# Kernel tuning notes

Hardware: AMD Instinct MI355X
Metric: run time of the kernel (lower is better)

The kernel has to match this reference:

```python
import jax, jax.numpy as jnp
import numpy as np

B, T, D, M = 64, 2048, 256, 20
UNIT = 2
RADIUS_FACTOR = 0.2
SIGMA_FACTOR = 0.2
KERNEL = 3
TOPK = 100
EPS = 1e-12


def setup_inputs() -> dict:
    key = jax.random.key(0)
    ks = jax.random.split(key, 10)
    x = jax.random.normal(ks[0], (B, T, D), jnp.float32)
    saliency = jax.random.normal(ks[1], (B, T), jnp.float32)
    # ground-truth boundaries in frame units, -1 start marks padding objects
    b0 = jax.random.uniform(ks[2], (B, M), minval=0.0, maxval=UNIT * (T - 100))
    length = jax.random.uniform(ks[3], (B, M), minval=UNIT * 2.0, maxval=UNIT * 100.0)
    b1 = jnp.minimum(b0 + length, float(UNIT * T))
    valid = jax.random.uniform(ks[4], (B, M)) < 0.8
    b0 = jnp.where(valid, b0, -1.0)
    boundary = jnp.stack([b0, b1], axis=-1)
    sc = 1.0 / np.sqrt(D)
    w_center = jax.random.normal(ks[5], (D, 1), jnp.float32) * sc
    w_window = jax.random.normal(ks[6], (D, 1), jnp.float32) * sc
    w_offset = jax.random.normal(ks[7], (D, 1), jnp.float32) * sc
    zb = jnp.zeros((1,), jnp.float32)
    return dict(x=x, w_center=w_center, b_center=zb, w_window=w_window, b_window=zb,
                w_offset=w_offset, b_offset=zb, saliency=saliency, boundary=boundary)


def _get_targets(boundary):
    # boundary: [B, M, 2] in frame units; vectorized version of the torch double loop
    b0 = boundary[..., 0]
    b1 = boundary[..., 1]
    valid = b0 != -1.0                                   # [B, M]
    b0c = b0 / UNIT
    b1c = (b1 - UNIT) / UNIT
    centers = jnp.minimum((b0c + b1c) * 0.5, T - 0.5)    # [B, M]
    windows = b1c - b0c                                   # [B, M]
    radius = (windows * RADIUS_FACTOR).astype(jnp.int32)  # trunc like .int()
    sigma = (radius.astype(jnp.float32) + 1.0) * SIGMA_FACTOR
    ci = centers.astype(jnp.int32)                        # [B, M]
    t = jnp.arange(T)
    d = t[None, None, :] - ci[..., None]                  # [B, M, T]
    g = jnp.exp(-(d.astype(jnp.float32) ** 2) / (2.0 * sigma[..., None] ** 2))
    inband = (jnp.abs(d) <= radius[..., None]) & valid[..., None]
    g = jnp.where(inband, g, 0.0)
    center_tgt = g.max(axis=1)                            # scatter-max over objects
    rows = jnp.arange(B)[:, None]
    idx = jnp.where(valid, ci, T)                         # out-of-range -> dropped
    z = jnp.zeros((B, T), jnp.float32)
    window_tgt = z.at[rows, idx].set(windows, mode='drop')
    offset_tgt = z.at[rows, idx].set(centers - ci.astype(jnp.float32), mode='drop')
    weight = z.at[rows, idx].set(1.0, mode='drop')
    avg_factor = valid.sum().astype(jnp.float32)
    return center_tgt, window_tgt, offset_tgt, weight, avg_factor


def _get_boundary(center_pred, window_pred, offset_pred):
    pad = (KERNEL - 1) // 2
    hmax = jax.lax.reduce_window(center_pred, -jnp.inf, jax.lax.max,
                                 (1, KERNEL), (1, 1), [(0, 0), (pad, pad)])
    cp = jnp.where(hmax == center_pred, center_pred, 0.0)
    scores, inds = jax.lax.top_k(cp, TOPK)                # [B, TOPK]
    off = jnp.maximum(jnp.take_along_axis(offset_pred, inds, axis=1), 0.0)
    center = inds.astype(jnp.float32) + off
    window = jnp.maximum(jnp.take_along_axis(window_pred, inds, axis=1), 0.0)
    lo = jnp.clip(center - window / 2, 0.0, T - 1.0) * UNIT
    hi = jnp.clip(center + window / 2, 0.0, T - 1.0) * UNIT + UNIT
    return jnp.stack([lo, hi, scores], axis=-1)           # [B, TOPK, 3]


def reference(x, w_center, b_center, w_window, b_window, w_offset, b_offset, saliency, boundary):
    mask = (saliency >= 0).astype(x.dtype)                # [B, T]
    center_pred = jax.nn.sigmoid(jnp.einsum('btd,do->bt', x, w_center) + b_center[0]) * mask
    window_pred = jnp.einsum('btd,do->bt', x, w_window) + b_window[0]
    offset_pred = jnp.einsum('btd,do->bt', x, w_offset) + b_offset[0]

    center_tgt, window_tgt, offset_tgt, weight, avg = _get_targets(boundary)

    # GaussianFocalLoss (alpha=2, gamma=4), weighted by mask, mean over avg_factor
    pos = (center_tgt == 1.0).astype(jnp.float32)
    pos_loss = -jnp.log(center_pred + EPS) * (1.0 - center_pred) ** 2 * pos
    neg_loss = -jnp.log(1.0 - center_pred + EPS) * center_pred ** 2 * (1.0 - center_tgt) ** 4
    center_loss = ((pos_loss + neg_loss) * mask).sum() / avg
    window_loss = 0.1 * (jnp.abs(window_pred - window_tgt) * weight).sum() / avg
    offset_loss = 1.0 * (jnp.abs(offset_pred - offset_tgt) * weight).sum() / avg

    boundary_out = _get_boundary(center_pred, window_pred, offset_pred)
    return (boundary_out, center_loss, window_loss, offset_loss)
```

## Files before the change

### kernel.cpp

```cpp
#include <hip/hip_runtime.h>
#include <math.h>

#define BB 64
#define TT 2048
#define DD 256
#define MM 20
#define TOPK_N 100
#define EPSF 1e-12f

__global__ __launch_bounds__(256) void preds_kernel(
    const float* __restrict__ x,
    const float* __restrict__ wc, const float* __restrict__ bc,
    const float* __restrict__ ww, const float* __restrict__ bw,
    const float* __restrict__ wo, const float* __restrict__ bo,
    const float* __restrict__ sal,
    float* __restrict__ cp, float* __restrict__ wp, float* __restrict__ op)
{
    const int lane = threadIdx.x & 63;
    const int waveg = blockIdx.x * 4 + (threadIdx.x >> 6);
    const int nwaves = gridDim.x * 4;

    const float4 wc4 = ((const float4*)wc)[lane];
    const float4 ww4 = ((const float4*)ww)[lane];
    const float4 wo4 = ((const float4*)wo)[lane];
    const float bcs = bc[0], bws = bw[0], bos = bo[0];

    for (int row = waveg; row < BB * TT; row += nwaves) {
        const float4 x4 = ((const float4*)(x + (size_t)row * DD))[lane];
        float sc = x4.x * wc4.x + x4.y * wc4.y + x4.z * wc4.z + x4.w * wc4.w;
        float sw = x4.x * ww4.x + x4.y * ww4.y + x4.z * ww4.z + x4.w * ww4.w;
        float so = x4.x * wo4.x + x4.y * wo4.y + x4.z * wo4.z + x4.w * wo4.w;
        #pragma unroll
        for (int m = 32; m >= 1; m >>= 1) {
            sc += __shfl_xor(sc, m, 64);
            sw += __shfl_xor(sw, m, 64);
            so += __shfl_xor(so, m, 64);
        }
        if (lane == 0) {
            const float mask = (sal[row] >= 0.0f) ? 1.0f : 0.0f;
            const float z = sc + bcs;
            const float s = 1.0f / (1.0f + expf(-z));
            cp[row] = s * mask;
            wp[row] = sw + bws;
            op[row] = so + bos;
        }
    }
}

__global__ __launch_bounds__(256) void targets_kernel(
    const float* __restrict__ boundary, const float* __restrict__ sal,
    const float* __restrict__ cp, const float* __restrict__ wp,
    const float* __restrict__ op, float* __restrict__ partials)
{
    __shared__ int   s_ci[MM];
    __shared__ float s_win[MM], s_off[MM], s_sig[MM];
    __shared__ int   s_rad[MM], s_valid[MM], s_last[MM];
    __shared__ float s_red[4][4];

    const int b = blockIdx.x;
    const int tid = threadIdx.x;

    if (tid < MM) {
        const float b0 = boundary[(b * MM + tid) * 2 + 0];
        const float b1 = boundary[(b * MM + tid) * 2 + 1];
        const int v = (b0 != -1.0f) ? 1 : 0;
        const float b0c = b0 * 0.5f;
        const float b1c = (b1 - 2.0f) * 0.5f;
        const float c = fminf((b0c + b1c) * 0.5f, (float)TT - 0.5f);
        const float w = b1c - b0c;
        const int r = (int)(w * 0.2f);
        const float sg = ((float)r + 1.0f) * 0.2f;
        const int ci = (int)c;
        s_ci[tid] = ci; s_win[tid] = w; s_off[tid] = c - (float)ci;
        s_sig[tid] = sg; s_rad[tid] = r; s_valid[tid] = v;
    }
    __syncthreads();
    if (tid < MM) {
        int last = s_valid[tid];
        if (last) {
            for (int m2 = tid + 1; m2 < MM; ++m2)
                if (s_valid[m2] && s_ci[m2] == s_ci[tid]) { last = 0; break; }
        }
        s_last[tid] = last;
    }
    __syncthreads();

    float cl = 0.0f, wl = 0.0f, ol = 0.0f, cnt = 0.0f;
    if (tid < MM) {
        if (s_valid[tid]) cnt = 1.0f;
        if (s_last[tid]) {
            const int t = s_ci[tid];
            wl = fabsf(wp[b * TT + t] - s_win[tid]);
            ol = fabsf(op[b * TT + t] - s_off[tid]);
        }
    }
    for (int t = tid; t < TT; t += 256) {
        float ctgt = 0.0f;
        for (int m = 0; m < MM; ++m) {
            if (!s_valid[m]) continue;
            const int d = t - s_ci[m];
            const int ad = d < 0 ? -d : d;
            if (ad <= s_rad[m]) {
                const float df = (float)d;
                const float sg = s_sig[m];
                const float g = expf(-(df * df) / (2.0f * sg * sg));
                ctgt = fmaxf(ctgt, g);
            }
        }
        const float p = cp[b * TT + t];
        const float mask = (sal[b * TT + t] >= 0.0f) ? 1.0f : 0.0f;
        const float pos = (ctgt == 1.0f) ? 1.0f : 0.0f;
        const float om = 1.0f - p;
        const float pl = -logf(p + EPSF) * om * om * pos;
        const float q = 1.0f - ctgt;
        const float q2 = q * q;
        const float nl = -logf(1.0f - p + EPSF) * p * p * (q2 * q2);
        cl += (pl + nl) * mask;
    }
    #pragma unroll
    for (int m = 32; m >= 1; m >>= 1) {
        cl  += __shfl_xor(cl,  m, 64);
        wl  += __shfl_xor(wl,  m, 64);
        ol  += __shfl_xor(ol,  m, 64);
        cnt += __shfl_xor(cnt, m, 64);
    }
    if ((tid & 63) == 0) {
        const int w = tid >> 6;
        s_red[w][0] = cl; s_red[w][1] = wl; s_red[w][2] = ol; s_red[w][3] = cnt;
    }
    __syncthreads();
    if (tid == 0) {
        float a = 0, b2 = 0, c = 0, d = 0;
        for (int w = 0; w < 4; ++w) {
            a += s_red[w][0]; b2 += s_red[w][1]; c += s_red[w][2]; d += s_red[w][3];
        }
        partials[b * 4 + 0] = a; partials[b * 4 + 1] = b2;
        partials[b * 4 + 2] = c; partials[b * 4 + 3] = d;
    }
}

__global__ void finalize_kernel(const float* __restrict__ partials, float* __restrict__ out)
{
    if (threadIdx.x == 0 && blockIdx.x == 0) {
        float cl = 0, wl = 0, ol = 0, cnt = 0;
        for (int i = 0; i < BB; ++i) {
            cl += partials[i * 4 + 0]; wl += partials[i * 4 + 1];
            ol += partials[i * 4 + 2]; cnt += partials[i * 4 + 3];
        }
        out[BB * TOPK_N * 3 + 0] = cl / cnt;
        out[BB * TOPK_N * 3 + 1] = 0.1f * wl / cnt;
        out[BB * TOPK_N * 3 + 2] = ol / cnt;
    }
}

__global__ __launch_bounds__(256) void topk_kernel(
    const float* __restrict__ cp, const float* __restrict__ wp,
    const float* __restrict__ op, float* __restrict__ out)
{
    __shared__ unsigned long long keys[TT];
    const int b = blockIdx.x;
    const int tid = threadIdx.x;
    const float* row = cp + b * TT;

    for (int t = tid; t < TT; t += 256) {
        const float p = row[t];
        const float l = (t > 0) ? row[t - 1] : -1.0f;
        const float r = (t < TT - 1) ? row[t + 1] : -1.0f;
        const float hm = fmaxf(p, fmaxf(l, r));
        const float v = (hm == p) ? p : 0.0f;
        keys[t] = ((unsigned long long)__float_as_uint(v) << 32)
                | (unsigned int)(0xFFFFFFFFu - (unsigned int)t);
    }
    __syncthreads();

    for (int k = 2; k <= TT; k <<= 1) {
        for (int j = k >> 1; j >= 1; j >>= 1) {
            for (int i = tid; i < TT; i += 256) {
                const int p = i ^ j;
                if (p > i) {
                    const bool desc = ((i & k) == 0);
                    const unsigned long long a = keys[i], bk = keys[p];
                    const bool sw = desc ? (a < bk) : (a > bk);
                    if (sw) { keys[i] = bk; keys[p] = a; }
                }
            }
            __syncthreads();
        }
    }

    if (tid < TOPK_N) {
        const unsigned long long kk = keys[tid];
        const int idx = (int)(0xFFFFFFFFu - (unsigned int)kk);
        const float score = __uint_as_float((unsigned int)(kk >> 32));
        const float off = fmaxf(op[b * TT + idx], 0.0f);
        const float center = (float)idx + off;
        const float win = fmaxf(wp[b * TT + idx], 0.0f);
        const float lo = fminf(fmaxf(center - win * 0.5f, 0.0f), (float)TT - 1.0f) * 2.0f;
        const float hi = fminf(fmaxf(center + win * 0.5f, 0.0f), (float)TT - 1.0f) * 2.0f + 2.0f;
        float* o = out + (b * TOPK_N + tid) * 3;
        o[0] = lo; o[1] = hi; o[2] = score;
    }
}

extern "C" void kernel_launch(void* const* d_in, const int* in_sizes, int n_in,
                              void* d_out, int out_size, void* d_ws, size_t ws_size,
                              hipStream_t stream) {
    const float* x   = (const float*)d_in[0];
    const float* wc  = (const float*)d_in[1];
    const float* bc  = (const float*)d_in[2];
    const float* ww  = (const float*)d_in[3];
    const float* bw  = (const float*)d_in[4];
    const float* wo  = (const float*)d_in[5];
    const float* bo  = (const float*)d_in[6];
    const float* sal = (const float*)d_in[7];
    const float* bnd = (const float*)d_in[8];
    float* out = (float*)d_out;

    float* ws = (float*)d_ws;
    float* cp = ws;
    float* wp = ws + BB * TT;
    float* op = ws + 2 * BB * TT;
    float* partials = ws + 3 * BB * TT;

    preds_kernel<<<4096, 256, 0, stream>>>(x, wc, bc, ww, bw, wo, bo, sal, cp, wp, op);
    targets_kernel<<<BB, 256, 0, stream>>>(bnd, sal, cp, wp, op, partials);
    finalize_kernel<<<1, 64, 0, stream>>>(partials, out);
    topk_kernel<<<BB, 256, 0, stream>>>(cp, wp, op, out);
}
```

Before: 294.8 us.

## Process four rows per wave in preds, fold finalize into topk, widen topk blocks

The projection kernel now assigns four rows per wavefront, with 16 lanes per row each loading four float4 chunks. This cuts the shuffle reduction from six steps to four and gives each lane more independent loads in flight. The separate finalize kernel is removed and its loss reduction moves into block 0 of the top-k kernel as a wave-level shuffle reduction, saving one launch. The top-k bitonic sort now runs with 512 threads per block instead of 256, halving the per-thread work in each sort pass.

```diff
diff --git a/kernel.cpp b/kernel.cpp
--- a/kernel.cpp
+++ b/kernel.cpp
@@ -17,29 +17,41 @@
     float* __restrict__ cp, float* __restrict__ wp, float* __restrict__ op)
 {
     const int lane = threadIdx.x & 63;
-    const int waveg = blockIdx.x * 4 + (threadIdx.x >> 6);
+    const int sub  = lane >> 4;
+    const int cg   = lane & 15;
+    const int waveg  = blockIdx.x * 4 + (threadIdx.x >> 6);
     const int nwaves = gridDim.x * 4;
 
-    const float4 wc4 = ((const float4*)wc)[lane];
-    const float4 ww4 = ((const float4*)ww)[lane];
-    const float4 wo4 = ((const float4*)wo)[lane];
+    float4 wc4[4], ww4[4], wo4[4];
+    #pragma unroll
+    for (int k = 0; k < 4; ++k) {
+        wc4[k] = ((const float4*)wc)[k * 16 + cg];
+        ww4[k] = ((const float4*)ww)[k * 16 + cg];
+        wo4[k] = ((const float4*)wo)[k * 16 + cg];
+    }
     const float bcs = bc[0], bws = bw[0], bos = bo[0];
 
-    for (int row = waveg; row < BB * TT; row += nwaves) {
-        const float4 x4 = ((const float4*)(x + (size_t)row * DD))[lane];
-        float sc = x4.x * wc4.x + x4.y * wc4.y + x4.z * wc4.z + x4.w * wc4.w;
-        float sw = x4.x * ww4.x + x4.y * ww4.y + x4.z * ww4.z + x4.w * ww4.w;
-        float so = x4.x * wo4.x + x4.y * wo4.y + x4.z * wo4.z + x4.w * wo4.w;
+    const int ngroups = BB * TT / 4;
+    for (int g = waveg; g < ngroups; g += nwaves) {
+        const int row = g * 4 + sub;
+        const float4* xr = (const float4*)(x + (size_t)row * DD);
+        float sc = 0.0f, sw = 0.0f, so = 0.0f;
         #pragma unroll
-        for (int m = 32; m >= 1; m >>= 1) {
+        for (int k = 0; k < 4; ++k) {
+            const float4 x4 = xr[k * 16 + cg];
+            sc += x4.x * wc4[k].x + x4.y * wc4[k].y + x4.z * wc4[k].z + x4.w * wc4[k].w;
+            sw += x4.x * ww4[k].x + x4.y * ww4[k].y + x4.z * ww4[k].z + x4.w * ww4[k].w;
+            so += x4.x * wo4[k].x + x4.y * wo4[k].y + x4.z * wo4[k].z + x4.w * wo4[k].w;
+        }
+        #pragma unroll
+        for (int m = 8; m >= 1; m >>= 1) {
             sc += __shfl_xor(sc, m, 64);
             sw += __shfl_xor(sw, m, 64);
             so += __shfl_xor(so, m, 64);
         }
-        if (lane == 0) {
+        if (cg == 0) {
             const float mask = (sal[row] >= 0.0f) ? 1.0f : 0.0f;
-            const float z = sc + bcs;
-            const float s = 1.0f / (1.0f + expf(-z));
+            const float s = 1.0f / (1.0f + expf(-(sc + bcs)));
             cp[row] = s * mask;
             wp[row] = sw + bws;
             op[row] = so + bos;
@@ -139,30 +151,17 @@
     }
 }
 
-__global__ void finalize_kernel(const float* __restrict__ partials, float* __restrict__ out)
-{
-    if (threadIdx.x == 0 && blockIdx.x == 0) {
-        float cl = 0, wl = 0, ol = 0, cnt = 0;
-        for (int i = 0; i < BB; ++i) {
-            cl += partials[i * 4 + 0]; wl += partials[i * 4 + 1];
-            ol += partials[i * 4 + 2]; cnt += partials[i * 4 + 3];
-        }
-        out[BB * TOPK_N * 3 + 0] = cl / cnt;
-        out[BB * TOPK_N * 3 + 1] = 0.1f * wl / cnt;
-        out[BB * TOPK_N * 3 + 2] = ol / cnt;
-    }
-}
-
-__global__ __launch_bounds__(256) void topk_kernel(
+__global__ __launch_bounds__(512) void topk_kernel(
     const float* __restrict__ cp, const float* __restrict__ wp,
-    const float* __restrict__ op, float* __restrict__ out)
+    const float* __restrict__ op, const float* __restrict__ partials,
+    float* __restrict__ out)
 {
     __shared__ unsigned long long keys[TT];
     const int b = blockIdx.x;
     const int tid = threadIdx.x;
     const float* row = cp + b * TT;
 
-    for (int t = tid; t < TT; t += 256) {
+    for (int t = tid; t < TT; t += 512) {
         const float p = row[t];
         const float l = (t > 0) ? row[t - 1] : -1.0f;
         const float r = (t < TT - 1) ? row[t + 1] : -1.0f;
@@ -175,7 +174,7 @@
 
     for (int k = 2; k <= TT; k <<= 1) {
         for (int j = k >> 1; j >= 1; j >>= 1) {
-            for (int i = tid; i < TT; i += 256) {
+            for (int i = tid; i < TT; i += 512) {
                 const int p = i ^ j;
                 if (p > i) {
                     const bool desc = ((i & k) == 0);
@@ -199,6 +198,25 @@
         const float hi = fminf(fmaxf(center + win * 0.5f, 0.0f), (float)TT - 1.0f) * 2.0f + 2.0f;
         float* o = out + (b * TOPK_N + tid) * 3;
         o[0] = lo; o[1] = hi; o[2] = score;
+    }
+
+    if (b == 0 && tid < 64) {
+        float cl  = partials[tid * 4 + 0];
+        float wl  = partials[tid * 4 + 1];
+        float ol  = partials[tid * 4 + 2];
+        float cnt = partials[tid * 4 + 3];
+        #pragma unroll
+        for (int m = 32; m >= 1; m >>= 1) {
+            cl  += __shfl_xor(cl,  m, 64);
+            wl  += __shfl_xor(wl,  m, 64);
+            ol  += __shfl_xor(ol,  m, 64);
+            cnt += __shfl_xor(cnt, m, 64);
+        }
+        if (tid == 0) {
+            out[BB * TOPK_N * 3 + 0] = cl / cnt;
+            out[BB * TOPK_N * 3 + 1] = 0.1f * wl / cnt;
+            out[BB * TOPK_N * 3 + 2] = ol / cnt;
+        }
     }
 }
 
@@ -222,8 +240,7 @@
     float* op = ws + 2 * BB * TT;
     float* partials = ws + 3 * BB * TT;
 
-    preds_kernel<<<4096, 256, 0, stream>>>(x, wc, bc, ww, bw, wo, bo, sal, cp, wp, op);
+    preds_kernel<<<2048, 256, 0, stream>>>(x, wc, bc, ww, bw, wo, bo, sal, cp, wp, op);
     targets_kernel<<<BB, 256, 0, stream>>>(bnd, sal, cp, wp, op, partials);
-    finalize_kernel<<<1, 64, 0, stream>>>(partials, out);
-    topk_kernel<<<BB, 256, 0, stream>>>(cp, wp, op, out);
-}
+    topk_kernel<<<BB, 512, 0, stream>>>(cp, wp, op, partials, out);
+}
```

Result: faster. 260.9 us (-11.5%).
